# Kernel tuning notes

Measured on AMD Instinct MI355X. Metric: run time of the kernel, lower is better.

Reference implementation:

```python
import jax, jax.numpy as jnp
import numpy as np

N = 200000          # nodes
E = 6_400_000       # edges (avg degree 32)
F = 128             # num_node_features
H = 16              # GCN hidden width (hard-coded in module)
MLP_H = 100         # lin1 width (hard-coded)
C = 27              # num_classes (SIDER labels)
G = 4096            # number of graphs in the batch


def setup_inputs() -> dict:
    key = jax.random.key(0)
    ks = jax.random.split(key, 12)
    x = jax.random.normal(ks[0], (N, F), dtype=jnp.float32)
    edge_index = jax.random.randint(ks[1], (2, E), 0, N, dtype=jnp.int64)
    batch_vec = jnp.sort(jax.random.randint(ks[2], (N,), 0, G, dtype=jnp.int64))
    s = 0.05
    W1 = jax.random.normal(ks[3], (F, H), dtype=jnp.float32) * s
    b1 = jnp.zeros((H,), jnp.float32)
    W2 = jax.random.normal(ks[4], (H, H), dtype=jnp.float32) * s
    b2 = jnp.zeros((H,), jnp.float32)
    Wl1 = jax.random.normal(ks[5], (H, MLP_H), dtype=jnp.float32) * s
    bl1 = jnp.zeros((MLP_H,), jnp.float32)
    Wl2 = jax.random.normal(ks[6], (MLP_H, C), dtype=jnp.float32) * s
    bl2 = jnp.zeros((C,), jnp.float32)
    return dict(x=x, edge_index=edge_index, batch_vec=batch_vec,
                W1=W1, b1=b1, W2=W2, b2=b2, Wl1=Wl1, bl1=bl1, Wl2=Wl2, bl2=bl2)


def reference(x, edge_index, batch_vec, W1, b1, W2, b2, Wl1, bl1, Wl2, bl2):
    # PyG GCNConv: add self-loops, symmetric D^-1/2 (A+I) D^-1/2 normalization.
    src, dst = edge_index[0], edge_index[1]
    loop = jnp.arange(N, dtype=edge_index.dtype)
    src_f = jnp.concatenate([src, loop])   # [E+N]
    dst_f = jnp.concatenate([dst, loop])
    deg = jax.ops.segment_sum(jnp.ones(E + N, jnp.float32), dst_f, num_segments=N)
    dinv = jax.lax.rsqrt(deg)              # deg >= 1 due to self-loops
    norm = dinv[src_f] * dinv[dst_f]       # [E+N]

    def gcn_conv(h, W, b):
        h = h @ W                                       # transform first (cheaper: H=16)
        msg = h[src_f] * norm[:, None]                  # gather + scale  [E+N, H]
        return jax.ops.segment_sum(msg, dst_f, num_segments=N) + b

    h = jax.nn.relu(gcn_conv(x, W1, b1))   # dropout: identity in eval mode
    h = gcn_conv(h, W2, b2)
    g = jax.ops.segment_sum(h, batch_vec, num_segments=G)  # global_add_pool [G,H]
    g = jax.nn.relu(g)
    g = jax.nn.relu(g @ Wl1 + bl1)
    return g @ Wl2 + bl2                   # logits [G, C]
```

## Files before the change

kernel.cpp:

```cpp
#include <hip/hip_runtime.h>
#include <hip/hip_bf16.h>

#define NNODES 200000
#define NEDGES 6400000
#define NFEAT  128
#define NH     16
#define NMLP   100
#define NCLS   27
#define NGRAPH 4096

#define BKTSH  10
#define BKTW   1024
#define NBKT   ((NNODES + BKTW - 1) / BKTW)
#define NBLKA  512
#define ABLK   1024
#define EPB    (NEDGES / NBLKA)
#define EPB4   (EPB / 4)
#define HSZ    (NBKT * NBLKA)
#define SCANB  1024
#define NSCAN2 ((HSZ + SCANB - 1) / SCANB)
#define CAP    34816

typedef int v4i __attribute__((ext_vector_type(4)));

__device__ __forceinline__ unsigned short f2bf(float f) {
    unsigned u = __float_as_uint(f);
    return (unsigned short)((u + 0x7FFF + ((u >> 16) & 1)) >> 16);
}
__device__ __forceinline__ float bf2f(unsigned short s) {
    return __uint_as_float(((unsigned)s) << 16);
}

__global__ __launch_bounds__(ABLK) void k_histA(const int* __restrict__ dst,
                                                int* __restrict__ H) {
    __shared__ int hist[NBKT];
    int tid = threadIdx.x, k = blockIdx.x;
    for (int b = tid; b < NBKT; b += ABLK) hist[b] = 0;
    __syncthreads();
    const v4i* d4 = (const v4i*)(dst + (size_t)k * EPB);
    #pragma unroll 2
    for (int q = tid; q < EPB4; q += ABLK) {
        v4i d = __builtin_nontemporal_load(d4 + q);
        atomicAdd(&hist[d.x >> BKTSH], 1);
        atomicAdd(&hist[d.y >> BKTSH], 1);
        atomicAdd(&hist[d.z >> BKTSH], 1);
        atomicAdd(&hist[d.w >> BKTSH], 1);
    }
    __syncthreads();
    for (int b = tid; b < NBKT; b += ABLK) H[b * NBLKA + k] = hist[b];
}

__global__ __launch_bounds__(256) void k_scan_part(const int* __restrict__ A,
                                                   int* __restrict__ bsum) {
    __shared__ int sd[256];
    int tid = threadIdx.x;
    int i0 = blockIdx.x * SCANB + tid * 4;
    int s = 0;
    #pragma unroll
    for (int u = 0; u < 4; ++u) {
        int i = i0 + u;
        if (i < HSZ) s += A[i];
    }
    sd[tid] = s;
    __syncthreads();
    for (int off = 128; off > 0; off >>= 1) {
        if (tid < off) sd[tid] += sd[tid + off];
        __syncthreads();
    }
    if (tid == 0) bsum[blockIdx.x] = sd[0];
}

__global__ __launch_bounds__(256) void k_scan_top(int* __restrict__ bsum,
                                                  float* __restrict__ G,
                                                  int* __restrict__ cipad) {
    float4* G4 = (float4*)G;
    int tid = threadIdx.x;
    #pragma unroll
    for (int t = 0; t < (NGRAPH * NH / 4) / 256; ++t)
        G4[tid + t * 256] = make_float4(0.f, 0.f, 0.f, 0.f);
    if (tid < 64) cipad[tid] = 0;

    __shared__ int sd[256];
    int i0 = tid * 4;
    int c[4];
    #pragma unroll
    for (int u = 0; u < 4; ++u) {
        int i = i0 + u;
        c[u] = (i < NSCAN2) ? bsum[i] : 0;
    }
    int mysum = c[0] + c[1] + c[2] + c[3];
    sd[tid] = mysum;
    __syncthreads();
    for (int off = 1; off < 256; off <<= 1) {
        int v = (tid >= off) ? sd[tid - off] : 0;
        __syncthreads();
        sd[tid] += v;
        __syncthreads();
    }
    int base = sd[tid] - mysum;
    #pragma unroll
    for (int u = 0; u < 4; ++u) {
        int i = i0 + u;
        if (i < NSCAN2) { bsum[i] = base; base += c[u]; }
    }
}

__global__ __launch_bounds__(256) void k_scan_final(int* __restrict__ A,
                                                    const int* __restrict__ bsum) {
    __shared__ int sd[256];
    int tid = threadIdx.x;
    int i0 = blockIdx.x * SCANB + tid * 4;
    int c[4];
    #pragma unroll
    for (int u = 0; u < 4; ++u) {
        int i = i0 + u;
        c[u] = (i < HSZ) ? A[i] : 0;
    }
    int mysum = c[0] + c[1] + c[2] + c[3];
    sd[tid] = mysum;
    __syncthreads();
    for (int off = 1; off < 256; off <<= 1) {
        int v = (tid >= off) ? sd[tid - off] : 0;
        __syncthreads();
        sd[tid] += v;
        __syncthreads();
    }
    int base = bsum[blockIdx.x] + sd[tid] - mysum;
    #pragma unroll
    for (int u = 0; u < 4; ++u) {
        int i = i0 + u;
        if (i < HSZ) { A[i] = base; base += c[u]; }
    }
}

__global__ __launch_bounds__(ABLK) void k_scatterA(const int* __restrict__ src,
                                                   const int* __restrict__ dst,
                                                   const int* __restrict__ S,
                                                   int* __restrict__ P) {
    __shared__ int cnt[NBKT];
    int tid = threadIdx.x, k = blockIdx.x;
    for (int b = tid; b < NBKT; b += ABLK) cnt[b] = S[b * NBLKA + k];
    __syncthreads();
    const v4i* d4 = (const v4i*)(dst + (size_t)k * EPB);
    const v4i* s4 = (const v4i*)(src + (size_t)k * EPB);
    #pragma unroll 2
    for (int q = tid; q < EPB4; q += ABLK) {
        v4i d = __builtin_nontemporal_load(d4 + q);
        v4i s = __builtin_nontemporal_load(s4 + q);
        int p0 = atomicAdd(&cnt[d.x >> BKTSH], 1);
        int p1 = atomicAdd(&cnt[d.y >> BKTSH], 1);
        int p2 = atomicAdd(&cnt[d.z >> BKTSH], 1);
        int p3 = atomicAdd(&cnt[d.w >> BKTSH], 1);
        P[p0] = ((d.x & (BKTW - 1)) << 18) | s.x;
        P[p1] = ((d.y & (BKTW - 1)) << 18) | s.y;
        P[p2] = ((d.z & (BKTW - 1)) << 18) | s.z;
        P[p3] = ((d.w & (BKTW - 1)) << 18) | s.w;
    }
}

__global__ __launch_bounds__(ABLK) void k_csrB(const int* __restrict__ P,
                                               const int* __restrict__ S,
                                               int* __restrict__ rp,
                                               float* __restrict__ dinv,
                                               int* __restrict__ colidx) {
    __shared__ int outl[CAP];
    __shared__ int deg[BKTW];
    __shared__ int wp[BKTW];
    __shared__ int sc[BKTW];
    __shared__ int se[2];
    int b = blockIdx.x, tid = threadIdx.x;
    if (tid == 0) {
        se[0] = S[b * NBLKA];
        se[1] = (b == NBKT - 1) ? NEDGES : S[(b + 1) * NBLKA];
    }
    deg[tid] = 0;
    __syncthreads();
    int start = se[0], end = se[1];

    for (int i = start + tid; i < end; i += ABLK)
        atomicAdd(&deg[P[i] >> 18], 1);
    __syncthreads();

    int myc = deg[tid];
    sc[tid] = myc;
    __syncthreads();
    for (int off = 1; off < BKTW; off <<= 1) {
        int v = (tid >= off) ? sc[tid - off] : 0;
        __syncthreads();
        sc[tid] += v;
        __syncthreads();
    }
    wp[tid] = start + sc[tid] - myc;
    int node = b * BKTW + tid;
    if (node < NNODES) {
        rp[node]   = wp[tid];
        dinv[node] = rsqrtf(1.f + (float)myc);
    }
    if (b == 0 && tid == 0) rp[NNODES] = NEDGES;
    __syncthreads();

    for (int i = start + tid; i < end; i += ABLK) {
        int v = P[i];
        int pos = atomicAdd(&wp[v >> 18], 1);
        int rel = pos - start;
        if (rel < CAP) outl[rel] = v & 0x3FFFF;
        else           colidx[pos] = v & 0x3FFFF;
    }
    __syncthreads();

    int cnt = end - start;
    if (cnt > CAP) cnt = CAP;
    for (int i = tid; i < cnt; i += ABLK)
        colidx[start + i] = outl[i];
}

#define GROWS 64
#define GPAD  129
__global__ __launch_bounds__(256) void k_gemm1(const float* __restrict__ x,
                                               const float* __restrict__ W1,
                                               const float* __restrict__ dinv,
                                               unsigned short* __restrict__ A1b) {
    __shared__ float xt[GROWS * GPAD];
    __shared__ float Ws[NFEAT * NH];
    int tid = threadIdx.x;
    int r0 = blockIdx.x * GROWS;

    #pragma unroll
    for (int t = 0; t < (NFEAT * NH) / 256; ++t)
        Ws[tid + t * 256] = W1[tid + t * 256];

    const float4* xg = (const float4*)(x + (size_t)r0 * NFEAT);
    #pragma unroll
    for (int t = 0; t < (GROWS * NFEAT / 4) / 256; ++t) {
        int fi = tid + t * 256;
        float4 v = xg[fi];
        int row = fi >> 5;
        int c4  = fi & 31;
        float* p = &xt[row * GPAD + c4 * 4];
        p[0] = v.x; p[1] = v.y; p[2] = v.z; p[3] = v.w;
    }
    __syncthreads();

    int r  = tid >> 2;
    int jq = tid & 3;
    float4 acc = make_float4(0.f, 0.f, 0.f, 0.f);
    #pragma unroll 8
    for (int k = 0; k < NFEAT; ++k) {
        float xv = xt[r * GPAD + k];
        float4 w = *(const float4*)&Ws[k * NH + jq * 4];
        acc.x += xv * w.x; acc.y += xv * w.y;
        acc.z += xv * w.z; acc.w += xv * w.w;
    }
    int n = r0 + r;
    float s = dinv[n];
    ushort4 o;
    o.x = f2bf(acc.x * s); o.y = f2bf(acc.y * s);
    o.z = f2bf(acc.z * s); o.w = f2bf(acc.w * s);
    *(ushort4*)&A1b[(size_t)n * NH + jq * 4] = o;
}

__global__ __launch_bounds__(256) void k_gather1(const unsigned short* __restrict__ A1b,
                                                 const int* __restrict__ rp,
                                                 const int* __restrict__ ci,
                                                 const float* __restrict__ dinv,
                                                 const float* __restrict__ b1,
                                                 const float* __restrict__ W2,
                                                 unsigned short* __restrict__ A2b) {
    __shared__ float W2s[NH * NH];
    __shared__ float b1s[NH];
    int tid = threadIdx.x;
    if (tid < NH * NH) W2s[tid] = W2[tid];
    if (tid < NH)      b1s[tid] = b1[tid];
    __syncthreads();

    int nl = tid >> 4, j = tid & 15;
    int n  = blockIdx.x * 16 + nl;
    int r0 = rp[n], r1 = rp[n + 1];

    float acc = bf2f(A1b[(size_t)n * NH + j]);
    int k = r0;
    for (; k + 16 <= r1; k += 16) {
        int   c[16];
        float v[16];
        #pragma unroll
        for (int u = 0; u < 16; ++u) c[u] = ci[k + u];
        #pragma unroll
        for (int u = 0; u < 16; ++u) v[u] = bf2f(A1b[(size_t)c[u] * NH + j]);
        #pragma unroll
        for (int u = 0; u < 16; ++u) acc += v[u];
    }
    if (k < r1) {
        int   c[16];
        float v[16];
        #pragma unroll
        for (int u = 0; u < 16; ++u) c[u] = ci[k + u];
        #pragma unroll
        for (int u = 0; u < 16; ++u) v[u] = bf2f(A1b[(size_t)c[u] * NH + j]);
        #pragma unroll
        for (int u = 0; u < 16; ++u) acc += (k + u < r1) ? v[u] : 0.f;
    }

    float h = fmaxf(acc * dinv[n] + b1s[j], 0.f);
    float o = 0.f;
    #pragma unroll
    for (int kk = 0; kk < NH; ++kk)
        o += __shfl(h, kk, 16) * W2s[kk * NH + j];
    A2b[(size_t)n * NH + j] = f2bf(o * dinv[n]);
}

__global__ __launch_bounds__(256) void k_gather2(const unsigned short* __restrict__ A2b,
                                                 const int* __restrict__ rp,
                                                 const int* __restrict__ ci,
                                                 const float* __restrict__ dinv,
                                                 const float* __restrict__ b2,
                                                 const int* __restrict__ batch,
                                                 float* __restrict__ G) {
    __shared__ float b2s[NH];
    int tid = threadIdx.x;
    if (tid < NH) b2s[tid] = b2[tid];
    __syncthreads();

    int nl = tid >> 4, j = tid & 15;
    int n  = blockIdx.x * 16 + nl;
    int r0 = rp[n], r1 = rp[n + 1];

    float acc = bf2f(A2b[(size_t)n * NH + j]);
    int k = r0;
    for (; k + 16 <= r1; k += 16) {
        int   c[16];
        float v[16];
        #pragma unroll
        for (int u = 0; u < 16; ++u) c[u] = ci[k + u];
        #pragma unroll
        for (int u = 0; u < 16; ++u) v[u] = bf2f(A2b[(size_t)c[u] * NH + j]);
        #pragma unroll
        for (int u = 0; u < 16; ++u) acc += v[u];
    }
    if (k < r1) {
        int   c[16];
        float v[16];
        #pragma unroll
        for (int u = 0; u < 16; ++u) c[u] = ci[k + u];
        #pragma unroll
        for (int u = 0; u < 16; ++u) v[u] = bf2f(A2b[(size_t)c[u] * NH + j]);
        #pragma unroll
        for (int u = 0; u < 16; ++u) acc += (k + u < r1) ? v[u] : 0.f;
    }

    float h2 = acc * dinv[n] + b2s[j];
    atomicAdd(&G[(size_t)batch[n] * NH + j], h2);
}

__global__ __launch_bounds__(128) void k_head(const float* __restrict__ G,
                                              const float* __restrict__ Wl1,
                                              const float* __restrict__ bl1,
                                              const float* __restrict__ Wl2,
                                              const float* __restrict__ bl2,
                                              float* __restrict__ out) {
    __shared__ float gv[NH];
    __shared__ float g1[NMLP];
    int g = blockIdx.x, tid = threadIdx.x;

    if (tid < NH) gv[tid] = fmaxf(G[(size_t)g * NH + tid], 0.f);
    __syncthreads();

    if (tid < NMLP) {
        float a = bl1[tid];
        #pragma unroll
        for (int k = 0; k < NH; ++k) a += gv[k] * Wl1[k * NMLP + tid];
        g1[tid] = fmaxf(a, 0.f);
    }
    __syncthreads();

    if (tid < NCLS) {
        float a = bl2[tid];
        for (int k = 0; k < NMLP; ++k) a += g1[k] * Wl2[k * NCLS + tid];
        out[(size_t)g * NCLS + tid] = a;
    }
}

extern "C" void kernel_launch(void* const* d_in, const int* in_sizes, int n_in,
                              void* d_out, int out_size, void* d_ws, size_t ws_size,
                              hipStream_t stream) {
    const float* x     = (const float*)d_in[0];
    const int*   edge  = (const int*)d_in[1];
    const int*   batch = (const int*)d_in[2];
    const float* W1    = (const float*)d_in[3];
    const float* b1    = (const float*)d_in[4];
    const float* W2    = (const float*)d_in[5];
    const float* b2    = (const float*)d_in[6];
    const float* Wl1   = (const float*)d_in[7];
    const float* bl1   = (const float*)d_in[8];
    const float* Wl2   = (const float*)d_in[9];
    const float* bl2   = (const float*)d_in[10];
    float*       out   = (float*)d_out;

    char* ws = (char*)d_ws;
    size_t cur = 0;
    auto alloc = [&](size_t bytes) {
        void* p = ws + cur;
        cur += (bytes + 255) & ~(size_t)255;
        return p;
    };
    int*   H      = (int*)  alloc((size_t)HSZ * 4);
    int*   bsum   = (int*)  alloc((size_t)NSCAN2 * 4);
    int*   P      = (int*)  alloc((size_t)NEDGES * 4);
    int*   colidx = (int*)  alloc((size_t)(NEDGES + 64) * 4);
    int*   rp     = (int*)  alloc((size_t)(NNODES + 1) * 4);
    float* dinv   = (float*)alloc((size_t)NNODES * 4);
    float* G      = (float*)alloc((size_t)NGRAPH * NH * 4);
    unsigned short* A1b = (unsigned short*)P;
    unsigned short* A2b = A1b + (size_t)NNODES * NH;

    const int* src = edge;
    const int* dst = edge + NEDGES;

    int nb_gemm = NNODES / GROWS;
    int nb_gath = NNODES / 16;

    k_histA     <<<NBLKA,  ABLK, 0, stream>>>(dst, H);
    k_scan_part <<<NSCAN2, 256, 0, stream>>>(H, bsum);
    k_scan_top  <<<1,      256, 0, stream>>>(bsum, G, colidx + NEDGES);
    k_scan_final<<<NSCAN2, 256, 0, stream>>>(H, bsum);
    k_scatterA  <<<NBLKA,  ABLK, 0, stream>>>(src, dst, H, P);
    k_csrB      <<<NBKT,   ABLK, 0, stream>>>(P, H, rp, dinv, colidx);
    k_gemm1     <<<nb_gemm, 256, 0, stream>>>(x, W1, dinv, A1b);
    k_gather1   <<<nb_gath, 256, 0, stream>>>(A1b, rp, colidx, dinv, b1, W2, A2b);
    k_gather2   <<<nb_gath, 256, 0, stream>>>(A2b, rp, colidx, dinv, b2, batch, G);
    k_head      <<<NGRAPH, 128, 0, stream>>>(G, Wl1, bl1, Wl2, bl2, out);
}
```

Baseline: 290.1 us.

## Split CSR by source half and gather in two grid-synchronized phases

The CSR build now sorts each node's neighbours into two segments by source index (below or above a split point) and stores two row pointers per node. The gather kernels become persistent-style grids of 1792 blocks, each handling 112 nodes. Every block first gathers from the lower half of the feature table, then waits at a spin barrier with a timeout, then gathers from the upper half. The aim is to keep the working set of the random feature gathers small enough to stay cache-resident. The cost is a global spin barrier that relies on all blocks being co-resident, with a timeout fallback, plus more row-pointer traffic.

```diff
diff --git a/kernel.cpp b/kernel.cpp
--- a/kernel.cpp
+++ b/kernel.cpp
@@ -21,6 +21,11 @@
 #define NSCAN2 ((HSZ + SCANB - 1) / SCANB)
 #define CAP    34816
 
+#define SPLIT  100000
+#define GBLK   1792
+#define NPB    112
+#define SPINMAX 2000
+
 typedef int v4i __attribute__((ext_vector_type(4)));
 
 __device__ __forceinline__ unsigned short f2bf(float f) {
@@ -72,13 +77,15 @@
 
 __global__ __launch_bounds__(256) void k_scan_top(int* __restrict__ bsum,
                                                   float* __restrict__ G,
-                                                  int* __restrict__ cipad) {
+                                                  int* __restrict__ cipad,
+                                                  int* __restrict__ bars) {
     float4* G4 = (float4*)G;
     int tid = threadIdx.x;
     #pragma unroll
     for (int t = 0; t < (NGRAPH * NH / 4) / 256; ++t)
         G4[tid + t * 256] = make_float4(0.f, 0.f, 0.f, 0.f);
     if (tid < 64) cipad[tid] = 0;
+    if (tid < 2)  bars[tid] = 0;
 
     __shared__ int sd[256];
     int i0 = tid * 4;
@@ -160,12 +167,12 @@
 
 __global__ __launch_bounds__(ABLK) void k_csrB(const int* __restrict__ P,
                                                const int* __restrict__ S,
-                                               int* __restrict__ rp,
+                                               int* __restrict__ rp2,
                                                float* __restrict__ dinv,
                                                int* __restrict__ colidx) {
     __shared__ int outl[CAP];
-    __shared__ int deg[BKTW];
-    __shared__ int wp[BKTW];
+    __shared__ int deg2[BKTW * 2];
+    __shared__ int wp2[BKTW * 2];
     __shared__ int sc[BKTW];
     __shared__ int se[2];
     int b = blockIdx.x, tid = threadIdx.x;
@@ -173,16 +180,20 @@
         se[0] = S[b * NBLKA];
         se[1] = (b == NBKT - 1) ? NEDGES : S[(b + 1) * NBLKA];
     }
-    deg[tid] = 0;
+    deg2[tid] = 0;
+    deg2[tid + BKTW] = 0;
     __syncthreads();
     int start = se[0], end = se[1];
 
-    for (int i = start + tid; i < end; i += ABLK)
-        atomicAdd(&deg[P[i] >> 18], 1);
-    __syncthreads();
-
-    int myc = deg[tid];
-    sc[tid] = myc;
+    for (int i = start + tid; i < end; i += ABLK) {
+        int v = P[i];
+        atomicAdd(&deg2[(v >> 18) * 2 + ((v & 0x3FFFF) >= SPLIT)], 1);
+    }
+    __syncthreads();
+
+    int c0 = deg2[tid * 2], c1 = deg2[tid * 2 + 1];
+    int mysum = c0 + c1;
+    sc[tid] = mysum;
     __syncthreads();
     for (int off = 1; off < BKTW; off <<= 1) {
         int v = (tid >= off) ? sc[tid - off] : 0;
@@ -190,21 +201,26 @@
         sc[tid] += v;
         __syncthreads();
     }
-    wp[tid] = start + sc[tid] - myc;
+    int p0 = start + sc[tid] - mysum;
+    int p1 = p0 + c0;
+    wp2[tid * 2] = p0;
+    wp2[tid * 2 + 1] = p1;
     int node = b * BKTW + tid;
     if (node < NNODES) {
-        rp[node]   = wp[tid];
-        dinv[node] = rsqrtf(1.f + (float)myc);
-    }
-    if (b == 0 && tid == 0) rp[NNODES] = NEDGES;
+        rp2[(size_t)node * 2]     = p0;
+        rp2[(size_t)node * 2 + 1] = p1;
+        dinv[node] = rsqrtf(1.f + (float)mysum);
+    }
+    if (b == 0 && tid == 0) rp2[2 * NNODES] = NEDGES;
     __syncthreads();
 
     for (int i = start + tid; i < end; i += ABLK) {
         int v = P[i];
-        int pos = atomicAdd(&wp[v >> 18], 1);
+        int s = v & 0x3FFFF;
+        int pos = atomicAdd(&wp2[(v >> 18) * 2 + (s >= SPLIT)], 1);
         int rel = pos - start;
-        if (rel < CAP) outl[rel] = v & 0x3FFFF;
-        else           colidx[pos] = v & 0x3FFFF;
+        if (rel < CAP) outl[rel] = s;
+        else           colidx[pos] = s;
     }
     __syncthreads();
 
@@ -259,13 +275,67 @@
     *(ushort4*)&A1b[(size_t)n * NH + jq * 4] = o;
 }
 
-__global__ __launch_bounds__(256) void k_gather1(const unsigned short* __restrict__ A1b,
-                                                 const int* __restrict__ rp,
-                                                 const int* __restrict__ ci,
-                                                 const float* __restrict__ dinv,
-                                                 const float* __restrict__ b1,
-                                                 const float* __restrict__ W2,
-                                                 unsigned short* __restrict__ A2b) {
+__device__ __forceinline__ void gather_phases(const unsigned short* __restrict__ Ab,
+                                              const int* __restrict__ rp2,
+                                              const int* __restrict__ ci,
+                                              int* __restrict__ bar,
+                                              int base, int nl, int j,
+                                              float acc[7]) {
+    #pragma unroll
+    for (int p = 0; p < 2; ++p) {
+        for (int r = 0; r < 7; ++r) {
+            int n = base + r * 16 + nl;
+            if (n >= NNODES) continue;
+            int k = rp2[(size_t)n * 2 + p];
+            int e = rp2[(size_t)n * 2 + p + 1];
+            if (p == (int)(n >= SPLIT))
+                acc[r] += bf2f(Ab[(size_t)n * NH + j]);
+            for (; k + 8 <= e; k += 8) {
+                int   c[8];
+                float v[8];
+                #pragma unroll
+                for (int u = 0; u < 8; ++u) c[u] = ci[k + u];
+                #pragma unroll
+                for (int u = 0; u < 8; ++u) v[u] = bf2f(Ab[(size_t)c[u] * NH + j]);
+                #pragma unroll
+                for (int u = 0; u < 8; ++u) acc[r] += v[u];
+            }
+            if (k < e) {
+                int   c[8];
+                float v[8];
+                #pragma unroll
+                for (int u = 0; u < 8; ++u) c[u] = ci[k + u];
+                #pragma unroll
+                for (int u = 0; u < 8; ++u) v[u] = bf2f(Ab[(size_t)c[u] * NH + j]);
+                #pragma unroll
+                for (int u = 0; u < 8; ++u) acc[r] += (k + u < e) ? v[u] : 0.f;
+            }
+        }
+        if (p == 0) {
+            __syncthreads();
+            if (threadIdx.x == 0) {
+                atomicAdd(bar, 1);
+                int t = 0;
+                while (__hip_atomic_load(bar, __ATOMIC_RELAXED,
+                                         __HIP_MEMORY_SCOPE_AGENT) < GBLK
+                       && t < SPINMAX) {
+                    __builtin_amdgcn_s_sleep(16);
+                    ++t;
+                }
+            }
+            __syncthreads();
+        }
+    }
+}
+
+__global__ __launch_bounds__(256, 8) void k_gatherR1(const unsigned short* __restrict__ A1b,
+                                                     const int* __restrict__ rp2,
+                                                     const int* __restrict__ ci,
+                                                     const float* __restrict__ dinv,
+                                                     const float* __restrict__ b1,
+                                                     const float* __restrict__ W2,
+                                                     unsigned short* __restrict__ A2b,
+                                                     int* __restrict__ bar) {
     __shared__ float W2s[NH * NH];
     __shared__ float b1s[NH];
     int tid = threadIdx.x;
@@ -274,81 +344,55 @@
     __syncthreads();
 
     int nl = tid >> 4, j = tid & 15;
-    int n  = blockIdx.x * 16 + nl;
-    int r0 = rp[n], r1 = rp[n + 1];
-
-    float acc = bf2f(A1b[(size_t)n * NH + j]);
-    int k = r0;
-    for (; k + 16 <= r1; k += 16) {
-        int   c[16];
-        float v[16];
+    int base = blockIdx.x * NPB;
+    float acc[7];
+    #pragma unroll
+    for (int r = 0; r < 7; ++r) acc[r] = 0.f;
+
+    gather_phases(A1b, rp2, ci, bar, base, nl, j, acc);
+
+    #pragma unroll
+    for (int r = 0; r < 7; ++r) {
+        int n = base + r * 16 + nl;
+        if (n >= NNODES) continue;
+        float dv = dinv[n];
+        float h = fmaxf(acc[r] * dv + b1s[j], 0.f);
+        float o = 0.f;
         #pragma unroll
-        for (int u = 0; u < 16; ++u) c[u] = ci[k + u];
-        #pragma unroll
-        for (int u = 0; u < 16; ++u) v[u] = bf2f(A1b[(size_t)c[u] * NH + j]);
-        #pragma unroll
-        for (int u = 0; u < 16; ++u) acc += v[u];
-    }
-    if (k < r1) {
-        int   c[16];
-        float v[16];
-        #pragma unroll
-        for (int u = 0; u < 16; ++u) c[u] = ci[k + u];
-        #pragma unroll
-        for (int u = 0; u < 16; ++u) v[u] = bf2f(A1b[(size_t)c[u] * NH + j]);
-        #pragma unroll
-        for (int u = 0; u < 16; ++u) acc += (k + u < r1) ? v[u] : 0.f;
-    }
-
-    float h = fmaxf(acc * dinv[n] + b1s[j], 0.f);
-    float o = 0.f;
-    #pragma unroll
-    for (int kk = 0; kk < NH; ++kk)
-        o += __shfl(h, kk, 16) * W2s[kk * NH + j];
-    A2b[(size_t)n * NH + j] = f2bf(o * dinv[n]);
-}
-
-__global__ __launch_bounds__(256) void k_gather2(const unsigned short* __restrict__ A2b,
-                                                 const int* __restrict__ rp,
-                                                 const int* __restrict__ ci,
-                                                 const float* __restrict__ dinv,
-                                                 const float* __restrict__ b2,
-                                                 const int* __restrict__ batch,
-                                                 float* __restrict__ G) {
+        for (int kk = 0; kk < NH; ++kk)
+            o += __shfl(h, kk, 16) * W2s[kk * NH + j];
+        __builtin_nontemporal_store(f2bf(o * dv), &A2b[(size_t)n * NH + j]);
+    }
+}
+
+__global__ __launch_bounds__(256, 8) void k_gatherR2(const unsigned short* __restrict__ A2b,
+                                                     const int* __restrict__ rp2,
+                                                     const int* __restrict__ ci,
+                                                     const float* __restrict__ dinv,
+                                                     const float* __restrict__ b2,
+                                                     const int* __restrict__ batch,
+                                                     float* __restrict__ G,
+                                                     int* __restrict__ bar) {
     __shared__ float b2s[NH];
     int tid = threadIdx.x;
     if (tid < NH) b2s[tid] = b2[tid];
     __syncthreads();
 
     int nl = tid >> 4, j = tid & 15;
-    int n  = blockIdx.x * 16 + nl;
-    int r0 = rp[n], r1 = rp[n + 1];
-
-    float acc = bf2f(A2b[(size_t)n * NH + j]);
-    int k = r0;
-    for (; k + 16 <= r1; k += 16) {
-        int   c[16];
-        float v[16];
-        #pragma unroll
-        for (int u = 0; u < 16; ++u) c[u] = ci[k + u];
-        #pragma unroll
-        for (int u = 0; u < 16; ++u) v[u] = bf2f(A2b[(size_t)c[u] * NH + j]);
-        #pragma unroll
-        for (int u = 0; u < 16; ++u) acc += v[u];
-    }
-    if (k < r1) {
-        int   c[16];
-        float v[16];
-        #pragma unroll
-        for (int u = 0; u < 16; ++u) c[u] = ci[k + u];
-        #pragma unroll
-        for (int u = 0; u < 16; ++u) v[u] = bf2f(A2b[(size_t)c[u] * NH + j]);
-        #pragma unroll
-        for (int u = 0; u < 16; ++u) acc += (k + u < r1) ? v[u] : 0.f;
-    }
-
-    float h2 = acc * dinv[n] + b2s[j];
-    atomicAdd(&G[(size_t)batch[n] * NH + j], h2);
+    int base = blockIdx.x * NPB;
+    float acc[7];
+    #pragma unroll
+    for (int r = 0; r < 7; ++r) acc[r] = 0.f;
+
+    gather_phases(A2b, rp2, ci, bar, base, nl, j, acc);
+
+    #pragma unroll
+    for (int r = 0; r < 7; ++r) {
+        int n = base + r * 16 + nl;
+        if (n >= NNODES) continue;
+        float h2 = acc[r] * dinv[n] + b2s[j];
+        atomicAdd(&G[(size_t)batch[n] * NH + j], h2);
+    }
 }
 
 __global__ __launch_bounds__(128) void k_head(const float* __restrict__ G,
@@ -406,9 +450,10 @@
     int*   bsum   = (int*)  alloc((size_t)NSCAN2 * 4);
     int*   P      = (int*)  alloc((size_t)NEDGES * 4);
     int*   colidx = (int*)  alloc((size_t)(NEDGES + 64) * 4);
-    int*   rp     = (int*)  alloc((size_t)(NNODES + 1) * 4);
+    int*   rp2    = (int*)  alloc((size_t)(2 * NNODES + 2) * 4);
     float* dinv   = (float*)alloc((size_t)NNODES * 4);
     float* G      = (float*)alloc((size_t)NGRAPH * NH * 4);
+    int*   bars   = (int*)  alloc(2 * 4);
     unsigned short* A1b = (unsigned short*)P;
     unsigned short* A2b = A1b + (size_t)NNODES * NH;
 
@@ -416,16 +461,15 @@
     const int* dst = edge + NEDGES;
 
     int nb_gemm = NNODES / GROWS;
-    int nb_gath = NNODES / 16;
 
     k_histA     <<<NBLKA,  ABLK, 0, stream>>>(dst, H);
     k_scan_part <<<NSCAN2, 256, 0, stream>>>(H, bsum);
-    k_scan_top  <<<1,      256, 0, stream>>>(bsum, G, colidx + NEDGES);
+    k_scan_top  <<<1,      256, 0, stream>>>(bsum, G, colidx + NEDGES, bars);
     k_scan_final<<<NSCAN2, 256, 0, stream>>>(H, bsum);
     k_scatterA  <<<NBLKA,  ABLK, 0, stream>>>(src, dst, H, P);
-    k_csrB      <<<NBKT,   ABLK, 0, stream>>>(P, H, rp, dinv, colidx);
+    k_csrB      <<<NBKT,   ABLK, 0, stream>>>(P, H, rp2, dinv, colidx);
     k_gemm1     <<<nb_gemm, 256, 0, stream>>>(x, W1, dinv, A1b);
-    k_gather1   <<<nb_gath, 256, 0, stream>>>(A1b, rp, colidx, dinv, b1, W2, A2b);
-    k_gather2   <<<nb_gath, 256, 0, stream>>>(A2b, rp, colidx, dinv, b2, batch, G);
+    k_gatherR1  <<<GBLK,   256, 0, stream>>>(A1b, rp2, colidx, dinv, b1, W2, A2b, bars + 0);
+    k_gatherR2  <<<GBLK,   256, 0, stream>>>(A2b, rp2, colidx, dinv, b2, batch, G, bars + 1);
     k_head      <<<NGRAPH, 128, 0, stream>>>(G, Wl1, bl1, Wl2, bl2, out);
 }
```

Result: slower. 543.6 us (+87.4%).
